# Performance work log

Hardware: AMD Instinct MI355X
Metric: run time of the kernel (lower is better)

## Reference

```python
import jax, jax.numpy as jnp
import numpy as np

B, T, D, FF, E = 4, 2048, 512, 2048, 8
TOP_K = 2
EPS = 0.01


def setup_inputs() -> dict:
    key = jax.random.key(0)
    ks = jax.random.split(key, 7)
    s = 0.02
    return {
        "x": jax.random.normal(ks[0], (B, T, D), dtype=jnp.float32),
        "Wg": jax.random.normal(ks[1], (D, E), dtype=jnp.float32) * s,
        "bg": jnp.zeros((E,), dtype=jnp.float32),
        "W1": jax.random.normal(ks[2], (E, D, FF), dtype=jnp.float32) * s,
        "b1": jnp.zeros((E, FF), dtype=jnp.float32),
        "W2": jax.random.normal(ks[3], (E, FF, D), dtype=jnp.float32) * s,
        "b2": jnp.zeros((E, D), dtype=jnp.float32),
    }


def reference(x, Wg, bg, W1, b1, W2, b2):
    b, t, d = x.shape
    e = Wg.shape[1]
    # Gating: softmax over experts, top-k selection, renormalize with eps.
    logits = jnp.einsum("btd,de->bte", x, Wg) + bg          # [B,T,E]
    gates = jax.nn.softmax(logits, axis=-1)
    vals, idx = jax.lax.top_k(gates, TOP_K)                  # [B,T,K]
    vals = vals / (jnp.sum(vals, axis=-1, keepdims=True) + EPS)
    # Per-token per-expert combine weight (scatter of top-k vals into E slots).
    w = jnp.sum(jax.nn.one_hot(idx, e, dtype=x.dtype) * vals[..., None], axis=-2)  # [B,T,E]
    w = w.reshape(-1, e)                                     # [N,E], N=B*T
    xf = x.reshape(-1, d)                                    # [N,D]
    # Per-expert FFN (Linear -> ReLU -> Linear); zero-weight tokens contribute 0,
    # matching the original's masked gather/scatter.
    h = jax.nn.relu(jnp.einsum("nd,edf->enf", xf, W1) + b1[:, None, :])  # [E,N,FF]
    y = jnp.einsum("enf,efd->end", h, W2) + b2[:, None, :]               # [E,N,D]
    out = jnp.einsum("ne,end->nd", w, y)                                 # [N,D]
    return out.reshape(b, t, d)
```

## Files before the change

kernel.cpp:

```cpp
#include <hip/hip_runtime.h>
#include <hip/hip_bf16.h>
#include <cstdint>

#define NTOK   8192
#define DDIM   512
#define FDIM   2048
#define NEXP   8
#define NSLOT  16384
#define MAXTILES 136

typedef __bf16 bf16;
typedef __bf16 bf16x8 __attribute__((ext_vector_type(8)));
typedef float  f32x4  __attribute__((ext_vector_type(4)));

typedef uint32_t __attribute__((address_space(1))) gu32;
typedef uint32_t __attribute__((address_space(3))) lu32;

__device__ __forceinline__ void gload16(const void* g, void* l) {
    __builtin_amdgcn_global_load_lds((const gu32*)(uintptr_t)g,
                                     (lu32*)(uintptr_t)l, 16, 0, 0);
}

__global__ __launch_bounds__(256)
void gating_kernel(const float* __restrict__ x, const float* __restrict__ Wg,
                   const float* __restrict__ bg, bf16* __restrict__ xb,
                   int* __restrict__ top_idx, float* __restrict__ top_w,
                   int* __restrict__ counts)
{
    __shared__ int cnt_s[NEXP];
    if (threadIdx.x < NEXP) cnt_s[threadIdx.x] = 0;
    __syncthreads();

    const int w = threadIdx.x >> 6;
    const int l = threadIdx.x & 63;
    const int gw = blockIdx.x * 4 + w;

    for (int n = gw; n < NTOK; n += 4096) {
        const float4* xp = (const float4*)(x + (size_t)n * DDIM + l * 8);
        float4 x0 = xp[0], x1 = xp[1];
        float xf[8] = {x0.x, x0.y, x0.z, x0.w, x1.x, x1.y, x1.z, x1.w};

        bf16x8 xv;
#pragma unroll
        for (int i = 0; i < 8; ++i) xv[i] = (bf16)xf[i];
        *(bf16x8*)(xb + (size_t)n * DDIM + l * 8) = xv;

        float acc[8] = {0.f,0.f,0.f,0.f,0.f,0.f,0.f,0.f};
#pragma unroll
        for (int i = 0; i < 8; ++i) {
            const float4* wp = (const float4*)(Wg + (size_t)(l * 8 + i) * NEXP);
            float4 wa = wp[0], wb = wp[1];
            acc[0] += xf[i] * wa.x; acc[1] += xf[i] * wa.y;
            acc[2] += xf[i] * wa.z; acc[3] += xf[i] * wa.w;
            acc[4] += xf[i] * wb.x; acc[5] += xf[i] * wb.y;
            acc[6] += xf[i] * wb.z; acc[7] += xf[i] * wb.w;
        }
#pragma unroll
        for (int m = 32; m >= 1; m >>= 1)
#pragma unroll
            for (int e = 0; e < 8; ++e)
                acc[e] += __shfl_xor(acc[e], m);

        if (l == 0) {
            float logit[8];
#pragma unroll
            for (int e = 0; e < 8; ++e) logit[e] = acc[e] + bg[e];
            float mx = logit[0];
#pragma unroll
            for (int e = 1; e < 8; ++e) mx = fmaxf(mx, logit[e]);
            float g[8], s = 0.f;
#pragma unroll
            for (int e = 0; e < 8; ++e) { g[e] = expf(logit[e] - mx); s += g[e]; }
            float inv = 1.f / s;
#pragma unroll
            for (int e = 0; e < 8; ++e) g[e] *= inv;
            int e0 = 0;
#pragma unroll
            for (int e = 1; e < 8; ++e) if (g[e] > g[e0]) e0 = e;
            int e1 = (e0 == 0) ? 1 : 0;
#pragma unroll
            for (int e = 0; e < 8; ++e) if (e != e0 && e != e1 && g[e] > g[e1]) e1 = e;
            float denom = g[e0] + g[e1] + 0.01f;
            top_idx[n * 2 + 0] = e0;
            top_idx[n * 2 + 1] = e1;
            top_w[n * 2 + 0] = g[e0] / denom;
            top_w[n * 2 + 1] = g[e1] / denom;
            atomicAdd(&cnt_s[e0], 1);
            atomicAdd(&cnt_s[e1], 1);
        }
    }
    __syncthreads();
    if (threadIdx.x < NEXP) atomicAdd(&counts[threadIdx.x], cnt_s[threadIdx.x]);
}

__global__ void scan_kernel(const int* __restrict__ counts, int* __restrict__ offsets,
                            int* __restrict__ tmap_e, int* __restrict__ tmap_rt,
                            int* __restrict__ ntiles, int* __restrict__ cursors)
{
    if (threadIdx.x == 0) {
        int off = 0;
        for (int e = 0; e < NEXP; ++e) { offsets[e] = off; off += counts[e]; cursors[e] = 0; }
        offsets[NEXP] = off;
        int t = 0;
        for (int e = 0; e < NEXP; ++e) {
            int nt = (counts[e] + 127) >> 7;
            for (int rt = 0; rt < nt; ++rt) { tmap_e[t] = e; tmap_rt[t] = rt; ++t; }
        }
        *ntiles = t;
    }
}

__global__ __launch_bounds__(256)
void scatter_kernel(const int* __restrict__ top_idx, const float* __restrict__ top_w,
                    const int* __restrict__ offsets, int* __restrict__ cursors,
                    int* __restrict__ slot_tok, float* __restrict__ slot_w,
                    int* __restrict__ pos)
{
    __shared__ int lcnt[NEXP];
    __shared__ int lbase[NEXP];
    const int t = threadIdx.x;
    if (t < NEXP) lcnt[t] = 0;
    __syncthreads();
    const int n = blockIdx.x * 256 + t;
    const int e0 = top_idx[n * 2 + 0];
    const int e1 = top_idx[n * 2 + 1];
    const int r0 = atomicAdd(&lcnt[e0], 1);
    const int r1 = atomicAdd(&lcnt[e1], 1);
    __syncthreads();
    if (t < NEXP) lbase[t] = atomicAdd(&cursors[t], lcnt[t]);
    __syncthreads();
    const int s0 = offsets[e0] + lbase[e0] + r0;
    const int s1 = offsets[e1] + lbase[e1] + r1;
    slot_tok[s0] = n; slot_w[s0] = top_w[n * 2 + 0]; pos[n * 2 + 0] = s0;
    slot_tok[s1] = n; slot_w[s1] = top_w[n * 2 + 1]; pos[n * 2 + 1] = s1;
}

__global__ __launch_bounds__(256)
void transpose_cvt(const float* __restrict__ src, bf16* __restrict__ dst, int R, int C)
{
    __shared__ bf16 tile[64][72];
    const size_t eo = (size_t)blockIdx.z * R * C;
    src += eo; dst += eo;
    const int c0 = blockIdx.x * 64, r0 = blockIdx.y * 64;
    const int tq = (threadIdx.x & 15) * 4;
    const int tr = threadIdx.x >> 4;
#pragma unroll
    for (int j = 0; j < 4; ++j) {
        const int r = tr + j * 16;
        float4 v = *(const float4*)(src + (size_t)(r0 + r) * C + c0 + tq);
        tile[tq + 0][r] = (bf16)v.x;
        tile[tq + 1][r] = (bf16)v.y;
        tile[tq + 2][r] = (bf16)v.z;
        tile[tq + 3][r] = (bf16)v.w;
    }
    __syncthreads();
    const int x8 = (threadIdx.x & 7) * 8;
    const int cr = threadIdx.x >> 3;
#pragma unroll
    for (int j = 0; j < 2; ++j) {
        const int c = cr + j * 32;
        *(bf16x8*)(dst + (size_t)(c0 + c) * R + r0 + x8) = *(const bf16x8*)&tile[c][x8];
    }
}

template<int KD, int ND, bool FIRST, int SK>
__global__ __launch_bounds__(512)
void moe_gemm(const bf16* __restrict__ Adata, const bf16* __restrict__ Bt,
              const float* __restrict__ bias, bf16* __restrict__ Out,
              const int* __restrict__ slot_tok, const int* __restrict__ offsets,
              const int* __restrict__ tmap_e, const int* __restrict__ tmap_rt,
              const int* __restrict__ ntiles)
{
    constexpr int NX  = ND / 256;
    constexpr int XD  = NX * SK;
    constexpr int NWG = XD * MAXTILES;
    constexpr int Q   = NWG / 8;

    const int orig = blockIdx.y * XD + blockIdx.x;
    const int work = (orig & 7) * Q + (orig >> 3);
    const int wy   = work / XD;
    const int rem  = work - wy * XD;
    const int wx   = rem % NX;
    const int ks   = rem / NX;
    if (wy >= *ntiles) return;

    const int e    = tmap_e[wy];
    const int rt   = tmap_rt[wy];
    const int row0 = offsets[e] + rt * 128;
    const int rowEnd = offsets[e + 1];
    const int nb   = wx * 256;
    const int kbase = ks * KD;

    __shared__ __align__(16) bf16 As[3 * 128 * 32];
    __shared__ __align__(16) bf16 Bs[3 * 256 * 32];

    const int t = threadIdx.x;
    const int w = t >> 6, l = t & 63;
    const int wm = w >> 2, wn = w & 3;

    const int rSub = l >> 2;
    const int colb = (l & 3) * 8;

    const int rA  = w * 16 + rSub;
    const int rB0 = (w * 2) * 16 + rSub;
    const int rB1 = (w * 2 + 1) * 16 + rSub;

    int srow = row0 + rA; if (srow >= NSLOT) srow = NSLOT - 1;
    const bf16* aSrc;
    if (FIRST) aSrc = Adata + (size_t)slot_tok[srow] * KD + colb;
    else       aSrc = Adata + (size_t)srow * (KD * SK) + kbase + colb;
    const bf16* bSrc0 = Bt + ((size_t)e * ND + nb + rB0) * (KD * SK) + kbase + colb;
    const bf16* bSrc1 = Bt + ((size_t)e * ND + nb + rB1) * (KD * SK) + kbase + colb;

    const int offA  = w * 512;
    const int offB0 = (w * 2) * 512;
    const int offB1 = (w * 2 + 1) * 512;

    f32x4 acc[4][4] = {};
    const int lr = l & 15;
    const int lk = (l >> 4) * 8;

    constexpr int NT = KD / 32;

    auto STAGE = [&](int buf, int k0) {
        gload16(aSrc  + k0, As + buf * 4096 + offA);
        gload16(bSrc0 + k0, Bs + buf * 8192 + offB0);
        gload16(bSrc1 + k0, Bs + buf * 8192 + offB1);
    };
    auto COMPUTE = [&](int buf) {
        const bf16* ab = As + buf * 4096;
        const bf16* bb = Bs + buf * 8192;
        bf16x8 aF[4], bF[4];
#pragma unroll
        for (int mi = 0; mi < 4; ++mi)
            aF[mi] = *(const bf16x8*)(ab + (wm * 64 + mi * 16 + lr) * 32 + lk);
#pragma unroll
        for (int nj = 0; nj < 4; ++nj)
            bF[nj] = *(const bf16x8*)(bb + (wn * 64 + nj * 16 + lr) * 32 + lk);
#pragma unroll
        for (int mi = 0; mi < 4; ++mi)
#pragma unroll
            for (int nj = 0; nj < 4; ++nj)
                acc[mi][nj] = __builtin_amdgcn_mfma_f32_16x16x32_bf16(
                    aF[mi], bF[nj], acc[mi][nj], 0, 0, 0);
    };

    STAGE(0, 0);
    STAGE(1, 32);
    STAGE(2, 64);
    __builtin_amdgcn_sched_barrier(0);

    int buf = 0;
    for (int t2 = 0; t2 < NT - 3; ++t2) {
        asm volatile("s_waitcnt vmcnt(6)" ::: "memory");
        __builtin_amdgcn_sched_barrier(0);
        __builtin_amdgcn_s_barrier();
        __builtin_amdgcn_sched_barrier(0);
        COMPUTE(buf);
        __builtin_amdgcn_s_barrier();
        __builtin_amdgcn_sched_barrier(0);
        STAGE(buf, (t2 + 3) * 32);
        __builtin_amdgcn_sched_barrier(0);
        buf = (buf == 2) ? 0 : buf + 1;
    }
    asm volatile("s_waitcnt vmcnt(6)" ::: "memory");
    __builtin_amdgcn_sched_barrier(0);
    __builtin_amdgcn_s_barrier();
    __builtin_amdgcn_sched_barrier(0);
    COMPUTE(buf);
    buf = (buf == 2) ? 0 : buf + 1;
    asm volatile("s_waitcnt vmcnt(3)" ::: "memory");
    __builtin_amdgcn_sched_barrier(0);
    __builtin_amdgcn_s_barrier();
    __builtin_amdgcn_sched_barrier(0);
    COMPUTE(buf);
    buf = (buf == 2) ? 0 : buf + 1;
    asm volatile("s_waitcnt vmcnt(0)" ::: "memory");
    __builtin_amdgcn_sched_barrier(0);
    __builtin_amdgcn_s_barrier();
    __builtin_amdgcn_sched_barrier(0);
    COMPUTE(buf);

    const int rowW = row0 + wm * 64;
    const int colW = nb + wn * 64;
    bf16* outBase = Out + (size_t)ks * NSLOT * ND;
#pragma unroll
    for (int mi = 0; mi < 4; ++mi) {
#pragma unroll
        for (int nj = 0; nj < 4; ++nj) {
#pragma unroll
            for (int r = 0; r < 4; ++r) {
                int row = rowW + mi * 16 + (l >> 4) * 4 + r;
                int col = colW + nj * 16 + lr;
                if (row < rowEnd) {
                    float v = acc[mi][nj][r];
                    if (FIRST)        v = fmaxf(v + bias[e * ND + col], 0.f);
                    else if (ks == 0) v = v + bias[e * ND + col];
                    outBase[(size_t)row * ND + col] = (bf16)v;
                }
            }
        }
    }
}

__global__ __launch_bounds__(256)
void combine_kernel(const bf16* __restrict__ Yg, const int* __restrict__ pos,
                    const float* __restrict__ slot_w, float* __restrict__ out)
{
    const int idx = blockIdx.x * 256 + threadIdx.x;
    const int n  = idx >> 6;
    const int d8 = (idx & 63) * 8;
    const int s0 = pos[n * 2 + 0], s1 = pos[n * 2 + 1];
    const float w0 = slot_w[s0], w1 = slot_w[s1];
    const bf16* y1 = Yg + (size_t)NSLOT * DDIM;
    bf16x8 a0 = *(const bf16x8*)(Yg + (size_t)s0 * DDIM + d8);
    bf16x8 a1 = *(const bf16x8*)(y1 + (size_t)s0 * DDIM + d8);
    bf16x8 b0 = *(const bf16x8*)(Yg + (size_t)s1 * DDIM + d8);
    bf16x8 b1 = *(const bf16x8*)(y1 + (size_t)s1 * DDIM + d8);
    float o[8];
#pragma unroll
    for (int j = 0; j < 8; ++j)
        o[j] = w0 * ((float)a0[j] + (float)a1[j]) + w1 * ((float)b0[j] + (float)b1[j]);
    float* op = out + (size_t)n * DDIM + d8;
    *(float4*)(op + 0) = make_float4(o[0], o[1], o[2], o[3]);
    *(float4*)(op + 4) = make_float4(o[4], o[5], o[6], o[7]);
}

extern "C" void kernel_launch(void* const* d_in, const int* in_sizes, int n_in,
                              void* d_out, int out_size, void* d_ws, size_t ws_size,
                              hipStream_t stream)
{
    (void)in_sizes; (void)n_in;
    const float* x  = (const float*)d_in[0];
    const float* Wg = (const float*)d_in[1];
    const float* bg = (const float*)d_in[2];
    const float* W1 = (const float*)d_in[3];
    const float* b1 = (const float*)d_in[4];
    const float* W2 = (const float*)d_in[5];
    const float* b2 = (const float*)d_in[6];
    float* out = (float*)d_out;

    uint8_t* ws = (uint8_t*)d_ws;
    size_t off = 0;
    auto alloc = [&](size_t bytes) -> void* {
        void* p = ws + off;
        off = (off + bytes + 255) & ~(size_t)255;
        return p;
    };
    bf16*  xb      = (bf16*)alloc((size_t)NTOK * DDIM * 2);
    bf16*  w1t     = (bf16*)alloc((size_t)NEXP * FDIM * DDIM * 2);
    bf16*  w2t     = (bf16*)alloc((size_t)NEXP * DDIM * FDIM * 2);
    bf16*  Hg      = (bf16*)alloc((size_t)NSLOT * FDIM * 2);
    bf16*  Yg      = (bf16*)alloc((size_t)2 * NSLOT * DDIM * 2);
    int*   counts  = (int*)alloc(NEXP * 4);
    int*   cursors = (int*)alloc(NEXP * 4);
    int*   offsets = (int*)alloc((NEXP + 1) * 4);
    int*   ntiles  = (int*)alloc(4);
    int*   tmap_e  = (int*)alloc(MAXTILES * 4);
    int*   tmap_rt = (int*)alloc(MAXTILES * 4);
    int*   top_idx = (int*)alloc((size_t)NTOK * 2 * 4);
    float* top_w   = (float*)alloc((size_t)NTOK * 2 * 4);
    int*   pos     = (int*)alloc((size_t)NTOK * 2 * 4);
    int*   slot_tok= (int*)alloc((size_t)NSLOT * 4);
    float* slot_w  = (float*)alloc((size_t)NSLOT * 4);

    if (ws_size < off) {
        hipMemsetAsync(d_out, 0, (size_t)out_size * 4, stream);
        return;
    }

    hipMemsetAsync(counts, 0, NEXP * 4, stream);

    gating_kernel<<<1024, 256, 0, stream>>>(x, Wg, bg, xb, top_idx, top_w, counts);
    scan_kernel<<<1, 64, 0, stream>>>(counts, offsets, tmap_e, tmap_rt, ntiles, cursors);
    scatter_kernel<<<NTOK / 256, 256, 0, stream>>>(top_idx, top_w, offsets, cursors,
                                                   slot_tok, slot_w, pos);
    transpose_cvt<<<dim3(FDIM / 64, DDIM / 64, NEXP), 256, 0, stream>>>(W1, w1t, DDIM, FDIM);
    transpose_cvt<<<dim3(DDIM / 64, FDIM / 64, NEXP), 256, 0, stream>>>(W2, w2t, FDIM, DDIM);

    moe_gemm<DDIM, FDIM, true, 1><<<dim3(FDIM / 256, MAXTILES), 512, 0, stream>>>(
        xb, w1t, b1, Hg, slot_tok, offsets, tmap_e, tmap_rt, ntiles);
    moe_gemm<FDIM / 2, DDIM, false, 2><<<dim3((DDIM / 256) * 2, MAXTILES), 512, 0, stream>>>(
        Hg, w2t, b2, Yg, slot_tok, offsets, tmap_e, tmap_rt, ntiles);

    combine_kernel<<<(NTOK * DDIM / 8) / 256, 256, 0, stream>>>(Yg, pos, slot_w, out);
}
```

Before: 204.5 us.

## Enlarge MoE GEMM tiles to 256x256x64 with XOR-swizzled LDS and double buffering

Each grouped-GEMM workgroup now covers 256 rows instead of 128, and each K step is 64 wide instead of 32. The LDS buffers use an XOR swizzle to avoid bank conflicts, and the pipeline drops from three buffers to two. The larger tile doubles per-wave accumulators (8x4 MFMA tiles) to raise data reuse per LDS load, and fewer tiles are scheduled per expert. The cost is higher register pressure (launch bounds set to one block), more padding waste on ragged expert tails, and fewer workgroups to fill the CUs.

```diff
diff --git a/kernel.cpp b/kernel.cpp
--- a/kernel.cpp
+++ b/kernel.cpp
@@ -7,7 +7,7 @@
 #define FDIM   2048
 #define NEXP   8
 #define NSLOT  16384
-#define MAXTILES 136
+#define MAXT256 72
 
 typedef __bf16 bf16;
 typedef __bf16 bf16x8 __attribute__((ext_vector_type(8)));
@@ -103,7 +103,7 @@
         offsets[NEXP] = off;
         int t = 0;
         for (int e = 0; e < NEXP; ++e) {
-            int nt = (counts[e] + 127) >> 7;
+            int nt = (counts[e] + 255) >> 8;
             for (int rt = 0; rt < nt; ++rt) { tmap_e[t] = e; tmap_rt[t] = rt; ++t; }
         }
         *ntiles = t;
@@ -164,7 +164,7 @@
 }
 
 template<int KD, int ND, bool FIRST, int SK>
-__global__ __launch_bounds__(512)
+__global__ __launch_bounds__(512, 1)
 void moe_gemm(const bf16* __restrict__ Adata, const bf16* __restrict__ Bt,
               const float* __restrict__ bias, bf16* __restrict__ Out,
               const int* __restrict__ slot_tok, const int* __restrict__ offsets,
@@ -173,8 +173,9 @@
 {
     constexpr int NX  = ND / 256;
     constexpr int XD  = NX * SK;
-    constexpr int NWG = XD * MAXTILES;
+    constexpr int NWG = XD * MAXT256;
     constexpr int Q   = NWG / 8;
+    constexpr int NT  = KD / 64;
 
     const int orig = blockIdx.y * XD + blockIdx.x;
     const int work = (orig & 7) * Q + (orig >> 3);
@@ -186,111 +187,101 @@
 
     const int e    = tmap_e[wy];
     const int rt   = tmap_rt[wy];
-    const int row0 = offsets[e] + rt * 128;
+    const int row0 = offsets[e] + rt * 256;
     const int rowEnd = offsets[e + 1];
     const int nb   = wx * 256;
     const int kbase = ks * KD;
 
-    __shared__ __align__(16) bf16 As[3 * 128 * 32];
-    __shared__ __align__(16) bf16 Bs[3 * 256 * 32];
+    __shared__ __align__(16) bf16 As[2 * 256 * 64];
+    __shared__ __align__(16) bf16 Bs[2 * 256 * 64];
 
     const int t = threadIdx.x;
     const int w = t >> 6, l = t & 63;
     const int wm = w >> 2, wn = w & 3;
-
-    const int rSub = l >> 2;
-    const int colb = (l & 3) * 8;
-
-    const int rA  = w * 16 + rSub;
-    const int rB0 = (w * 2) * 16 + rSub;
-    const int rB1 = (w * 2 + 1) * 16 + rSub;
-
-    int srow = row0 + rA; if (srow >= NSLOT) srow = NSLOT - 1;
-    const bf16* aSrc;
-    if (FIRST) aSrc = Adata + (size_t)slot_tok[srow] * KD + colb;
-    else       aSrc = Adata + (size_t)srow * (KD * SK) + kbase + colb;
-    const bf16* bSrc0 = Bt + ((size_t)e * ND + nb + rB0) * (KD * SK) + kbase + colb;
-    const bf16* bSrc1 = Bt + ((size_t)e * ND + nb + rB1) * (KD * SK) + kbase + colb;
-
-    const int offA  = w * 512;
-    const int offB0 = (w * 2) * 512;
-    const int offB1 = (w * 2 + 1) * 512;
-
-    f32x4 acc[4][4] = {};
     const int lr = l & 15;
-    const int lk = (l >> 4) * 8;
-
-    constexpr int NT = KD / 32;
+    const int sl = l >> 4;
+
+    const int srow_sub = t >> 3;
+    const int scol = (((t & 7) ^ (srow_sub & 7)) * 8);
+
+    const bf16* aSrcJ[4];
+    const bf16* bSrcJ[4];
+#pragma unroll
+    for (int j = 0; j < 4; ++j) {
+        const int r = j * 64 + srow_sub;
+        int sr = row0 + r; if (sr >= NSLOT) sr = NSLOT - 1;
+        if (FIRST) aSrcJ[j] = Adata + (size_t)slot_tok[sr] * (KD * SK) + kbase + scol;
+        else       aSrcJ[j] = Adata + (size_t)sr * (KD * SK) + kbase + scol;
+        bSrcJ[j] = Bt + ((size_t)e * ND + nb + r) * (KD * SK) + kbase + scol;
+    }
+
+    f32x4 acc[8][4] = {};
 
     auto STAGE = [&](int buf, int k0) {
-        gload16(aSrc  + k0, As + buf * 4096 + offA);
-        gload16(bSrc0 + k0, Bs + buf * 8192 + offB0);
-        gload16(bSrc1 + k0, Bs + buf * 8192 + offB1);
+#pragma unroll
+        for (int j = 0; j < 4; ++j) {
+            gload16(aSrcJ[j] + k0, As + buf * 16384 + j * 4096 + w * 512);
+            gload16(bSrcJ[j] + k0, Bs + buf * 16384 + j * 4096 + w * 512);
+        }
     };
     auto COMPUTE = [&](int buf) {
-        const bf16* ab = As + buf * 4096;
-        const bf16* bb = Bs + buf * 8192;
-        bf16x8 aF[4], bF[4];
-#pragma unroll
-        for (int mi = 0; mi < 4; ++mi)
-            aF[mi] = *(const bf16x8*)(ab + (wm * 64 + mi * 16 + lr) * 32 + lk);
-#pragma unroll
-        for (int nj = 0; nj < 4; ++nj)
-            bF[nj] = *(const bf16x8*)(bb + (wn * 64 + nj * 16 + lr) * 32 + lk);
-#pragma unroll
-        for (int mi = 0; mi < 4; ++mi)
+        const bf16* ab = As + buf * 16384;
+        const bf16* bb = Bs + buf * 16384;
+#pragma unroll
+        for (int kk = 0; kk < 2; ++kk) {
+            const int phys = ((kk * 4 + sl) ^ (lr & 7)) * 8;
+            bf16x8 aF[8], bF[4];
+#pragma unroll
+            for (int mi = 0; mi < 8; ++mi)
+                aF[mi] = *(const bf16x8*)(ab + (wm * 128 + mi * 16 + lr) * 64 + phys);
 #pragma unroll
             for (int nj = 0; nj < 4; ++nj)
-                acc[mi][nj] = __builtin_amdgcn_mfma_f32_16x16x32_bf16(
-                    aF[mi], bF[nj], acc[mi][nj], 0, 0, 0);
+                bF[nj] = *(const bf16x8*)(bb + (wn * 64 + nj * 16 + lr) * 64 + phys);
+#pragma unroll
+            for (int mi = 0; mi < 8; ++mi)
+#pragma unroll
+                for (int nj = 0; nj < 4; ++nj)
+                    acc[mi][nj] = __builtin_amdgcn_mfma_f32_16x16x32_bf16(
+                        aF[mi], bF[nj], acc[mi][nj], 0, 0, 0);
+        }
     };
 
     STAGE(0, 0);
-    STAGE(1, 32);
-    STAGE(2, 64);
-    __builtin_amdgcn_sched_barrier(0);
-
-    int buf = 0;
-    for (int t2 = 0; t2 < NT - 3; ++t2) {
-        asm volatile("s_waitcnt vmcnt(6)" ::: "memory");
+    STAGE(1, 64);
+    __builtin_amdgcn_sched_barrier(0);
+
+    for (int t2 = 0; t2 < NT - 2; ++t2) {
+        asm volatile("s_waitcnt vmcnt(8)" ::: "memory");
         __builtin_amdgcn_sched_barrier(0);
         __builtin_amdgcn_s_barrier();
         __builtin_amdgcn_sched_barrier(0);
-        COMPUTE(buf);
+        COMPUTE(t2 & 1);
         __builtin_amdgcn_s_barrier();
         __builtin_amdgcn_sched_barrier(0);
-        STAGE(buf, (t2 + 3) * 32);
+        STAGE(t2 & 1, (t2 + 2) * 64);
         __builtin_amdgcn_sched_barrier(0);
-        buf = (buf == 2) ? 0 : buf + 1;
-    }
-    asm volatile("s_waitcnt vmcnt(6)" ::: "memory");
+    }
+    asm volatile("s_waitcnt vmcnt(8)" ::: "memory");
     __builtin_amdgcn_sched_barrier(0);
     __builtin_amdgcn_s_barrier();
     __builtin_amdgcn_sched_barrier(0);
-    COMPUTE(buf);
-    buf = (buf == 2) ? 0 : buf + 1;
-    asm volatile("s_waitcnt vmcnt(3)" ::: "memory");
+    COMPUTE(NT & 1);
+    asm volatile("s_waitcnt vmcnt(0)" ::: "memory");
     __builtin_amdgcn_sched_barrier(0);
     __builtin_amdgcn_s_barrier();
     __builtin_amdgcn_sched_barrier(0);
-    COMPUTE(buf);
-    buf = (buf == 2) ? 0 : buf + 1;
-    asm volatile("s_waitcnt vmcnt(0)" ::: "memory");
-    __builtin_amdgcn_sched_barrier(0);
-    __builtin_amdgcn_s_barrier();
-    __builtin_amdgcn_sched_barrier(0);
-    COMPUTE(buf);
-
-    const int rowW = row0 + wm * 64;
+    COMPUTE((NT - 1) & 1);
+
+    const int rowW = row0 + wm * 128;
     const int colW = nb + wn * 64;
     bf16* outBase = Out + (size_t)ks * NSLOT * ND;
 #pragma unroll
-    for (int mi = 0; mi < 4; ++mi) {
+    for (int mi = 0; mi < 8; ++mi) {
 #pragma unroll
         for (int nj = 0; nj < 4; ++nj) {
 #pragma unroll
             for (int r = 0; r < 4; ++r) {
-                int row = rowW + mi * 16 + (l >> 4) * 4 + r;
+                int row = rowW + mi * 16 + sl * 4 + r;
                 int col = colW + nj * 16 + lr;
                 if (row < rowEnd) {
                     float v = acc[mi][nj][r];
@@ -356,8 +347,8 @@
     int*   cursors = (int*)alloc(NEXP * 4);
     int*   offsets = (int*)alloc((NEXP + 1) * 4);
     int*   ntiles  = (int*)alloc(4);
-    int*   tmap_e  = (int*)alloc(MAXTILES * 4);
-    int*   tmap_rt = (int*)alloc(MAXTILES * 4);
+    int*   tmap_e  = (int*)alloc(MAXT256 * 4);
+    int*   tmap_rt = (int*)alloc(MAXT256 * 4);
     int*   top_idx = (int*)alloc((size_t)NTOK * 2 * 4);
     float* top_w   = (float*)alloc((size_t)NTOK * 2 * 4);
     int*   pos     = (int*)alloc((size_t)NTOK * 2 * 4);
@@ -378,9 +369,9 @@
     transpose_cvt<<<dim3(FDIM / 64, DDIM / 64, NEXP), 256, 0, stream>>>(W1, w1t, DDIM, FDIM);
     transpose_cvt<<<dim3(DDIM / 64, FDIM / 64, NEXP), 256, 0, stream>>>(W2, w2t, FDIM, DDIM);
 
-    moe_gemm<DDIM, FDIM, true, 1><<<dim3(FDIM / 256, MAXTILES), 512, 0, stream>>>(
+    moe_gemm<DDIM, FDIM, true, 1><<<dim3(FDIM / 256, MAXT256), 512, 0, stream>>>(
         xb, w1t, b1, Hg, slot_tok, offsets, tmap_e, tmap_rt, ntiles);
-    moe_gemm<FDIM / 2, DDIM, false, 2><<<dim3((DDIM / 256) * 2, MAXTILES), 512, 0, stream>>>(
+    moe_gemm<FDIM / 2, DDIM, false, 2><<<dim3((DDIM / 256) * 2, MAXT256), 512, 0, stream>>>(
         Hg, w2t, b2, Yg, slot_tok, offsets, tmap_e, tmap_rt, ntiles);
 
     combine_kernel<<<(NTOK * DDIM / 8) / 256, 256, 0, stream>>>(Yg, pos, slot_w, out);
```

Result: slower. 240.5 us (+17.6%).
